# Kernel optimization log

Measured on AMD Instinct MI355X. Metric: run time of the kernel, lower is better.

## Reference

```python
import jax, jax.numpy as jnp
import numpy as np
from jax import lax

B, S, D = 2, 4096, 1024
E, H, K = 8, 2816, 2  # hidden_dim 4096 -> int(2*4096/3)=2730 -> round up to multiple_of 256 -> 2816


def setup_inputs() -> dict:
    key = jax.random.key(0)
    ks = jax.random.split(key, 5)
    scale = 0.02
    return {
        "x": jax.random.normal(ks[0], (B, S, D), dtype=jnp.float32),
        "router_w": jax.random.normal(ks[1], (E, D), dtype=jnp.float32) * scale,
        "w1": jax.random.normal(ks[2], (E, D, H), dtype=jnp.float32) * scale,
        "w2": jax.random.normal(ks[3], (E, H, D), dtype=jnp.float32) * scale,
        "w3": jax.random.normal(ks[4], (E, D, H), dtype=jnp.float32) * scale,
        "top_k": K,
    }


def reference(x, router_w, w1, w2, w3, top_k):
    b, s, d = x.shape
    e = router_w.shape[0]
    xf = x.reshape(-1, d)                                # [T, D]
    logits = xf @ router_w.T                             # [T, E]
    vals, idx = lax.top_k(logits, top_k)                 # [T, K]
    rw = jax.nn.softmax(vals.astype(jnp.float32), axis=-1).astype(x.dtype)  # [T, K]
    # combine[t, e] = routing weight of expert e for token t (0 if not selected)
    combine = jnp.sum(jax.nn.one_hot(idx, e, dtype=x.dtype) * rw[..., None], axis=1)  # [T, E]

    def body(acc, ew):
        w1e, w2e, w3e, ce = ew                           # [D,H], [H,D], [D,H], [T]
        h = jax.nn.silu(xf @ w1e) * (xf @ w3e)           # SwiGLU FFN, [T, H]
        return acc + (h @ w2e) * ce[:, None], None

    out, _ = lax.scan(body, jnp.zeros_like(xf), (w1, w2, w3, combine.T))
    return out.reshape(b, s, d)
```

## Files before the change

### kernel.cpp

```cpp
#include <hip/hip_runtime.h>
#include <stdint.h>

#define T_TOK 8192
#define DIM   1024
#define NE    8
#define NH    2816
#define NROWS (T_TOK*2)

typedef __attribute__((ext_vector_type(8))) __bf16 bf16x8;
typedef __attribute__((ext_vector_type(4))) float  f32x4;

typedef __attribute__((address_space(1))) const unsigned int g_as1;
typedef __attribute__((address_space(3))) unsigned int l_as3;
#define GLL(g, l) __builtin_amdgcn_global_load_lds((g_as1*)(g), (l_as3*)(l), 16, 0, 0)

__device__ __forceinline__ unsigned short f2bf(float f){
  union { float f; uint32_t u; } v; v.f = f;
  uint32_t r = (v.u + 0x7FFFu + ((v.u >> 16) & 1u)) >> 16;
  return (unsigned short)r;
}


__global__ void init_k(int* counts, int* cursor){
  int i = threadIdx.x;
  if (i < NE){ counts[i] = 0; cursor[i] = 0; }
}

__global__ void zero_out_k(float4* __restrict__ out){
  int i = blockIdx.x*blockDim.x + threadIdx.x;
  const int n4 = T_TOK*DIM/4;
  const float4 z = make_float4(0.f,0.f,0.f,0.f);
  for (; i < n4; i += gridDim.x*blockDim.x) out[i] = z;
}

__global__ void cvt_k(const float* __restrict__ x, unsigned short* __restrict__ xbf){
  int i = blockIdx.x*blockDim.x + threadIdx.x;
  const int total = T_TOK*DIM/8;
  for (; i < total; i += gridDim.x*blockDim.x){
    const float4 a = *(const float4*)(x + (size_t)i*8);
    const float4 b = *(const float4*)(x + (size_t)i*8 + 4);
    ushort4 lo = make_ushort4(f2bf(a.x), f2bf(a.y), f2bf(a.z), f2bf(a.w));
    ushort4 hi = make_ushort4(f2bf(b.x), f2bf(b.y), f2bf(b.z), f2bf(b.w));
    *(ushort4*)(xbf + (size_t)i*8)     = lo;
    *(ushort4*)(xbf + (size_t)i*8 + 4) = hi;
  }
}

__global__ __launch_bounds__(256) void transp_k(const float* __restrict__ in,
    unsigned short* __restrict__ outp, int R, int C)
{
  __shared__ unsigned short Tl[64*68];
  const int r0 = blockIdx.x*64, c0 = blockIdx.y*64;
  const size_t mbase = (size_t)blockIdx.z * (size_t)R * (size_t)C;
  const float* ip = in + mbase;
  unsigned short* op = outp + mbase;
  const int t = threadIdx.x;
  #pragma unroll
  for (int i=0;i<4;i++){
    const int r  = (t>>4) + i*16;
    const int cq = t & 15;
    const float4 v = *(const float4*)(ip + (size_t)(r0+r)*C + c0 + cq*4);
    Tl[(cq*4+0)*68 + r] = f2bf(v.x);
    Tl[(cq*4+1)*68 + r] = f2bf(v.y);
    Tl[(cq*4+2)*68 + r] = f2bf(v.z);
    Tl[(cq*4+3)*68 + r] = f2bf(v.w);
  }
  __syncthreads();
  #pragma unroll
  for (int i=0;i<4;i++){
    const int idx = i*1024 + t*4;
    const int c = idx>>6, r = idx&63;
    const ushort4 v = *(const ushort4*)&Tl[c*68 + r];
    *(ushort4*)(op + (size_t)(c0+c)*R + r0 + r) = v;
  }
}


__global__ void router_k(const float* __restrict__ x, const float* __restrict__ rw,
                         int* __restrict__ topk_e, float* __restrict__ topk_w,
                         int* __restrict__ counts){
  const int t = blockIdx.x;
  const int l = threadIdx.x;
  const float* xr = x + (size_t)t * DIM;
  float acc[NE];
  #pragma unroll
  for (int e=0;e<NE;e++) acc[e] = 0.f;
  #pragma unroll
  for (int i=0;i<DIM/64;i++){
    float xv = xr[l + 64*i];
    #pragma unroll
    for (int e=0;e<NE;e++) acc[e] += xv * rw[e*DIM + l + 64*i];
  }
  #pragma unroll
  for (int e=0;e<NE;e++){
    float v = acc[e];
    #pragma unroll
    for (int off=32; off; off>>=1) v += __shfl_xor(v, off);
    acc[e] = v;
  }
  if (l == 0){
    int e0 = 0; float v0 = acc[0];
    #pragma unroll
    for (int e=1;e<NE;e++) if (acc[e] > v0){ v0 = acc[e]; e0 = e; }
    int e1 = -1; float v1 = -1e30f;
    #pragma unroll
    for (int e=0;e<NE;e++) if (e != e0 && acc[e] > v1){ v1 = acc[e]; e1 = e; }
    float ex = __expf(v1 - v0);
    float s  = 1.f + ex;
    topk_e[t*2]   = e0;  topk_e[t*2+1] = e1;
    topk_w[t*2]   = 1.f/s; topk_w[t*2+1] = ex/s;
    atomicAdd(&counts[e0], 1);
    atomicAdd(&counts[e1], 1);
  }
}

__global__ void prefix_k(const int* __restrict__ counts, int* __restrict__ offs){
  if (threadIdx.x == 0 && blockIdx.x == 0){
    int s = 0;
    for (int e=0;e<NE;e++){ offs[e] = s; s += counts[e]; }
  }
}

__global__ void scatter_k(const int* __restrict__ topk_e, const float* __restrict__ topk_w,
                          const int* __restrict__ offs, int* __restrict__ cursor,
                          int* __restrict__ row_tok, float* __restrict__ row_w){
  int t = blockIdx.x*blockDim.x + threadIdx.x;
  if (t >= T_TOK) return;
  #pragma unroll
  for (int k=0;k<2;k++){
    int e = topk_e[t*2+k];
    int p = atomicAdd(&cursor[e], 1);
    int flat = offs[e] + p;
    row_tok[flat] = t;
    row_w[flat]   = topk_w[t*2+k];
  }
}


__global__ __launch_bounds__(512,2) void gemm1_bf(
    const unsigned short* __restrict__ xbf,
    const unsigned short* __restrict__ w1t, const unsigned short* __restrict__ w3t,
    unsigned short* __restrict__ hbuf,
    const int* __restrict__ row_tok,
    const int* __restrict__ counts, const int* __restrict__ offs)
{
  __shared__ unsigned short Al [2][128*32];
  __shared__ unsigned short B1l[2][128*32];
  __shared__ unsigned short B3l[2][128*32];

  const int e   = blockIdx.y >> 6;
  const int rb  = blockIdx.y & 63;
  const int cnt = counts[e];
  const int row0 = rb * 128;
  if (row0 >= cnt) return;
  const int nv   = min(128, cnt - row0);
  const int base = offs[e] + row0;
  const int h0   = blockIdx.x * 128;

  const int t  = threadIdx.x;
  const int srow = t >> 2, sch = t & 3;
  const int tok = row_tok[base + min(srow, nv-1)];
  const unsigned short* asrc = xbf + (size_t)tok*DIM + sch*8;
  const unsigned short* b1s  = w1t + ((size_t)(e*NH + h0 + srow))*DIM + sch*8;
  const unsigned short* b3s  = w3t + ((size_t)(e*NH + h0 + srow))*DIM + sch*8;
  const int lo = t*16;

  const int wid = t >> 6, l = t & 63;
  const int wr = wid >> 2, wc = wid & 3;
  const int lr = l & 15,  lk = l >> 4;

  f32x4 acc1[4][2], acc3[4][2];
  #pragma unroll
  for (int m=0;m<4;m++)
    #pragma unroll
    for (int n=0;n<2;n++){ acc1[m][n] = (f32x4)0.f; acc3[m][n] = (f32x4)0.f; }

  GLL(asrc, (char*)Al [0] + lo);
  GLL(b1s,  (char*)B1l[0] + lo);
  GLL(b3s,  (char*)B3l[0] + lo);
  __syncthreads();

  for (int kk=0; kk<DIM/32; ++kk){
    const int cur = kk & 1;
    if (kk < DIM/32 - 1){
      const int k1 = (kk+1)*32;
      GLL(asrc + k1, (char*)Al [cur^1] + lo);
      GLL(b1s  + k1, (char*)B1l[cur^1] + lo);
      GLL(b3s  + k1, (char*)B3l[cur^1] + lo);
    }
    bf16x8 a[4], b1[2], b3[2];
    #pragma unroll
    for (int m=0;m<4;m++) a[m] = *(const bf16x8*)&Al[cur][(wr*64 + m*16 + lr)*32 + lk*8];
    #pragma unroll
    for (int n=0;n<2;n++){
      b1[n] = *(const bf16x8*)&B1l[cur][(wc*32 + n*16 + lr)*32 + lk*8];
      b3[n] = *(const bf16x8*)&B3l[cur][(wc*32 + n*16 + lr)*32 + lk*8];
    }
    #pragma unroll
    for (int m=0;m<4;m++)
      #pragma unroll
      for (int n=0;n<2;n++){
        acc1[m][n] = __builtin_amdgcn_mfma_f32_16x16x32_bf16(a[m], b1[n], acc1[m][n], 0,0,0);
        acc3[m][n] = __builtin_amdgcn_mfma_f32_16x16x32_bf16(a[m], b3[n], acc3[m][n], 0,0,0);
      }
    __syncthreads();
  }

  #pragma unroll
  for (int m=0;m<4;m++){
    #pragma unroll
    for (int i=0;i<4;i++){
      const int r = wr*64 + m*16 + lk*4 + i;
      if (r < nv){
        const size_t rowbase = (size_t)(base + r) * NH;
        #pragma unroll
        for (int n=0;n<2;n++){
          float z  = acc1[m][n][i];
          float p3 = acc3[m][n][i];
          float hv = (z / (1.f + __expf(-z))) * p3;
          hbuf[rowbase + h0 + wc*32 + n*16 + lr] = f2bf(hv);
        }
      }
    }
  }
}

__global__ __launch_bounds__(512,2) void gemm2_bf(
    const unsigned short* __restrict__ hbuf,
    const unsigned short* __restrict__ w2t,
    float* __restrict__ out,
    const int* __restrict__ row_tok, const float* __restrict__ row_w,
    const int* __restrict__ counts, const int* __restrict__ offs)
{
  __shared__ unsigned short Al[2][128*32];
  __shared__ unsigned short Bl[2][128*32];

  const int e   = blockIdx.y >> 6;
  const int rb  = blockIdx.y & 63;
  const int cnt = counts[e];
  const int row0 = rb * 128;
  if (row0 >= cnt) return;
  const int nv   = min(128, cnt - row0);
  const int base = offs[e] + row0;
  const int d0   = blockIdx.x * 128;

  const int t  = threadIdx.x;
  const int srow = t >> 2, sch = t & 3;
  const unsigned short* asrc = hbuf + (size_t)(base + min(srow, nv-1))*NH + sch*8;
  const unsigned short* bs   = w2t + ((size_t)(e*DIM + d0 + srow))*NH + sch*8;
  const int lo = t*16;

  const int wid = t >> 6, l = t & 63;
  const int wr = wid >> 2, wc = wid & 3;
  const int lr = l & 15,  lk = l >> 4;

  f32x4 acc[4][2];
  #pragma unroll
  for (int m=0;m<4;m++)
    #pragma unroll
    for (int n=0;n<2;n++) acc[m][n] = (f32x4)0.f;

  GLL(asrc, (char*)Al[0] + lo);
  GLL(bs,   (char*)Bl[0] + lo);
  __syncthreads();

  for (int kk=0; kk<NH/32; ++kk){
    const int cur = kk & 1;
    if (kk < NH/32 - 1){
      const int k1 = (kk+1)*32;
      GLL(asrc + k1, (char*)Al[cur^1] + lo);
      GLL(bs   + k1, (char*)Bl[cur^1] + lo);
    }
    bf16x8 a[4], b[2];
    #pragma unroll
    for (int m=0;m<4;m++) a[m] = *(const bf16x8*)&Al[cur][(wr*64 + m*16 + lr)*32 + lk*8];
    #pragma unroll
    for (int n=0;n<2;n++)  b[n] = *(const bf16x8*)&Bl[cur][(wc*32 + n*16 + lr)*32 + lk*8];
    #pragma unroll
    for (int m=0;m<4;m++)
      #pragma unroll
      for (int n=0;n<2;n++)
        acc[m][n] = __builtin_amdgcn_mfma_f32_16x16x32_bf16(a[m], b[n], acc[m][n], 0,0,0);
    __syncthreads();
  }

  #pragma unroll
  for (int m=0;m<4;m++){
    #pragma unroll
    for (int i=0;i<4;i++){
      const int r = wr*64 + m*16 + lk*4 + i;
      if (r < nv){
        const int flat = base + r;
        const int tok  = row_tok[flat];
        const float wgt = row_w[flat];
        float* orow = out + (size_t)tok * DIM + d0 + wc*32;
        #pragma unroll
        for (int n=0;n<2;n++)
          atomicAdd(&orow[n*16 + lr], acc[m][n][i] * wgt);
      }
    }
  }
}


__global__ __launch_bounds__(256) void gemm1_k(
    const unsigned short* __restrict__ xbf,
    const float* __restrict__ w1, const float* __restrict__ w3,
    unsigned short* __restrict__ hbuf,
    const int* __restrict__ row_tok,
    const int* __restrict__ counts, const int* __restrict__ offs)
{
  __shared__ unsigned short Al [128*32];
  __shared__ unsigned short B1l[128*32];
  __shared__ unsigned short B3l[128*32];
  const int e   = blockIdx.y >> 6;
  const int rb  = blockIdx.y & 63;
  const int cnt = counts[e];
  const int row0 = rb * 128;
  if (row0 >= cnt) return;
  const int nv   = min(128, cnt - row0);
  const int base = offs[e] + row0;
  const int h0   = blockIdx.x * 128;
  const int t  = threadIdx.x;
  const int ar0 = t >> 2;
  const int ac  = t & 3;
  const int tok0 = row_tok[base + min(ar0,      nv-1)];
  const int tok1 = row_tok[base + min(ar0 + 64, nv-1)];
  const size_t asrc0 = (size_t)tok0 * DIM + ac*8;
  const size_t asrc1 = (size_t)tok1 * DIM + ac*8;
  const int dg = t >> 5;
  const int hq = t & 31;
  const float* w1p = w1 + (size_t)e * DIM * NH + (size_t)(h0 + hq*4);
  const float* w3p = w3 + (size_t)e * DIM * NH + (size_t)(h0 + hq*4);
  const int wid = t >> 6, l = t & 63;
  const int wr = wid >> 1, wc = wid & 1;
  const int lr = l & 15,  lk = l >> 4;
  f32x4 acc1[4][4], acc3[4][4];
  #pragma unroll
  for (int m=0;m<4;m++)
    #pragma unroll
    for (int n=0;n<4;n++){ acc1[m][n] = (f32x4)0.f; acc3[m][n] = (f32x4)0.f; }
  for (int kk=0; kk<DIM/32; ++kk){
    const int k0 = kk*32;
    __syncthreads();
    *(uint4*)&Al[ar0*32 + ac*8]      = *(const uint4*)(xbf + asrc0 + k0);
    *(uint4*)&Al[(ar0+64)*32 + ac*8] = *(const uint4*)(xbf + asrc1 + k0);
    {
      const float4 f0 = *(const float4*)(w1p + (size_t)(k0 + dg*4 + 0)*NH);
      const float4 f1 = *(const float4*)(w1p + (size_t)(k0 + dg*4 + 1)*NH);
      const float4 f2 = *(const float4*)(w1p + (size_t)(k0 + dg*4 + 2)*NH);
      const float4 f3 = *(const float4*)(w1p + (size_t)(k0 + dg*4 + 3)*NH);
      const float* p0=(const float*)&f0; const float* p1=(const float*)&f1;
      const float* p2=(const float*)&f2; const float* p3=(const float*)&f3;
      #pragma unroll
      for (int j=0;j<4;j++){
        ushort4 pk = make_ushort4(f2bf(p0[j]), f2bf(p1[j]), f2bf(p2[j]), f2bf(p3[j]));
        *(ushort4*)&B1l[(hq*4+j)*32 + dg*4] = pk;
      }
      const float4 g0 = *(const float4*)(w3p + (size_t)(k0 + dg*4 + 0)*NH);
      const float4 g1 = *(const float4*)(w3p + (size_t)(k0 + dg*4 + 1)*NH);
      const float4 g2 = *(const float4*)(w3p + (size_t)(k0 + dg*4 + 2)*NH);
      const float4 g3 = *(const float4*)(w3p + (size_t)(k0 + dg*4 + 3)*NH);
      const float* q0=(const float*)&g0; const float* q1=(const float*)&g1;
      const float* q2=(const float*)&g2; const float* q3=(const float*)&g3;
      #pragma unroll
      for (int j=0;j<4;j++){
        ushort4 pk = make_ushort4(f2bf(q0[j]), f2bf(q1[j]), f2bf(q2[j]), f2bf(q3[j]));
        *(ushort4*)&B3l[(hq*4+j)*32 + dg*4] = pk;
      }
    }
    __syncthreads();
    bf16x8 a[4], b1[4], b3[4];
    #pragma unroll
    for (int m=0;m<4;m++) a[m] = *(const bf16x8*)&Al[(wr*64 + m*16 + lr)*32 + lk*8];
    #pragma unroll
    for (int n=0;n<4;n++){
      b1[n] = *(const bf16x8*)&B1l[(wc*64 + n*16 + lr)*32 + lk*8];
      b3[n] = *(const bf16x8*)&B3l[(wc*64 + n*16 + lr)*32 + lk*8];
    }
    #pragma unroll
    for (int m=0;m<4;m++)
      #pragma unroll
      for (int n=0;n<4;n++){
        acc1[m][n] = __builtin_amdgcn_mfma_f32_16x16x32_bf16(a[m], b1[n], acc1[m][n], 0,0,0);
        acc3[m][n] = __builtin_amdgcn_mfma_f32_16x16x32_bf16(a[m], b3[n], acc3[m][n], 0,0,0);
      }
  }
  #pragma unroll
  for (int m=0;m<4;m++){
    #pragma unroll
    for (int i=0;i<4;i++){
      const int r = wr*64 + m*16 + lk*4 + i;
      if (r < nv){
        const size_t rowbase = (size_t)(base + r) * NH;
        #pragma unroll
        for (int n=0;n<4;n++){
          float z  = acc1[m][n][i];
          float p3 = acc3[m][n][i];
          float hv = (z / (1.f + __expf(-z))) * p3;
          hbuf[rowbase + h0 + wc*64 + n*16 + lr] = f2bf(hv);
        }
      }
    }
  }
}

__global__ __launch_bounds__(256) void gemm2_k(
    const unsigned short* __restrict__ hbuf,
    const float* __restrict__ w2,
    float* __restrict__ out,
    const int* __restrict__ row_tok, const float* __restrict__ row_w,
    const int* __restrict__ counts, const int* __restrict__ offs)
{
  __shared__ unsigned short Al[128*32];
  __shared__ unsigned short Bl[128*32];
  const int e   = blockIdx.y >> 6;
  const int rb  = blockIdx.y & 63;
  const int cnt = counts[e];
  const int row0 = rb * 128;
  if (row0 >= cnt) return;
  const int nv   = min(128, cnt - row0);
  const int base = offs[e] + row0;
  const int d0   = blockIdx.x * 128;
  const int t  = threadIdx.x;
  const int ar0 = t >> 2;
  const int ac  = t & 3;
  const size_t asrc0 = (size_t)(base + min(ar0,      nv-1)) * NH + ac*8;
  const size_t asrc1 = (size_t)(base + min(ar0 + 64, nv-1)) * NH + ac*8;
  const int dg = t >> 5;
  const int hq = t & 31;
  const float* w2p = w2 + (size_t)e * NH * DIM + (size_t)(d0 + hq*4);
  const int wid = t >> 6, l = t & 63;
  const int wr = wid >> 1, wc = wid & 1;
  const int lr = l & 15,  lk = l >> 4;
  f32x4 acc[4][4];
  #pragma unroll
  for (int m=0;m<4;m++)
    #pragma unroll
    for (int n=0;n<4;n++) acc[m][n] = (f32x4)0.f;
  for (int kk=0; kk<NH/32; ++kk){
    const int k0 = kk*32;
    __syncthreads();
    *(uint4*)&Al[ar0*32 + ac*8]      = *(const uint4*)(hbuf + asrc0 + k0);
    *(uint4*)&Al[(ar0+64)*32 + ac*8] = *(const uint4*)(hbuf + asrc1 + k0);
    {
      const float4 f0 = *(const float4*)(w2p + (size_t)(k0 + dg*4 + 0)*DIM);
      const float4 f1 = *(const float4*)(w2p + (size_t)(k0 + dg*4 + 1)*DIM);
      const float4 f2 = *(const float4*)(w2p + (size_t)(k0 + dg*4 + 2)*DIM);
      const float4 f3 = *(const float4*)(w2p + (size_t)(k0 + dg*4 + 3)*DIM);
      const float* p0=(const float*)&f0; const float* p1=(const float*)&f1;
      const float* p2=(const float*)&f2; const float* p3=(const float*)&f3;
      #pragma unroll
      for (int j=0;j<4;j++){
        ushort4 pk = make_ushort4(f2bf(p0[j]), f2bf(p1[j]), f2bf(p2[j]), f2bf(p3[j]));
        *(ushort4*)&Bl[(hq*4+j)*32 + dg*4] = pk;
      }
    }
    __syncthreads();
    bf16x8 a[4], b[4];
    #pragma unroll
    for (int m=0;m<4;m++) a[m] = *(const bf16x8*)&Al[(wr*64 + m*16 + lr)*32 + lk*8];
    #pragma unroll
    for (int n=0;n<4;n++)  b[n] = *(const bf16x8*)&Bl[(wc*64 + n*16 + lr)*32 + lk*8];
    #pragma unroll
    for (int m=0;m<4;m++)
      #pragma unroll
      for (int n=0;n<4;n++)
        acc[m][n] = __builtin_amdgcn_mfma_f32_16x16x32_bf16(a[m], b[n], acc[m][n], 0,0,0);
  }
  #pragma unroll
  for (int m=0;m<4;m++){
    #pragma unroll
    for (int i=0;i<4;i++){
      const int r = wr*64 + m*16 + lk*4 + i;
      if (r < nv){
        const int flat = base + r;
        const int tok  = row_tok[flat];
        const float wgt = row_w[flat];
        float* orow = out + (size_t)tok * DIM + d0 + wc*64;
        #pragma unroll
        for (int n=0;n<4;n++)
          atomicAdd(&orow[n*16 + lr], acc[m][n][i] * wgt);
      }
    }
  }
}


extern "C" void kernel_launch(void* const* d_in, const int* in_sizes, int n_in,
                              void* d_out, int out_size, void* d_ws, size_t ws_size,
                              hipStream_t stream) {
  (void)in_sizes; (void)n_in; (void)out_size;
  const float* x   = (const float*)d_in[0];
  const float* rw  = (const float*)d_in[1];
  const float* w1  = (const float*)d_in[2];
  const float* w2  = (const float*)d_in[3];
  const float* w3  = (const float*)d_in[4];
  float* out = (float*)d_out;
  char* ws = (char*)d_ws;

  const size_t SZ_XBF  = (size_t)T_TOK*DIM*2;
  const size_t SZ_HBUF = (size_t)NROWS*NH*2;
  const size_t SZ_WT   = (size_t)NE*NH*DIM*2;
  const size_t SZ_SMALL = (size_t)NROWS*4*2 + (size_t)T_TOK*2*4*2 + 3*64*4 + 4096;
  const size_t NEED_FAST = SZ_XBF + SZ_HBUF + 2*SZ_WT + SZ_SMALL;

  if (ws_size >= NEED_FAST) {
    size_t off = 0;
    unsigned short* xbf  = (unsigned short*)(ws + off); off += SZ_XBF;
    unsigned short* hbuf = (unsigned short*)(ws + off); off += SZ_HBUF;
    unsigned short* w1t  = (unsigned short*)(ws + off); off += SZ_WT;
    unsigned short* w3t  = (unsigned short*)(ws + off); off += SZ_WT;
    unsigned short* w2t  = w1t;
    int*   row_tok = (int*)  (ws + off); off += NROWS*4;
    float* row_w   = (float*)(ws + off); off += NROWS*4;
    int*   topk_e  = (int*)  (ws + off); off += T_TOK*2*4;
    float* topk_w  = (float*)(ws + off); off += T_TOK*2*4;
    int*   counts  = (int*)  (ws + off); off += 64;
    int*   offs    = (int*)  (ws + off); off += 64;
    int*   cursor  = (int*)  (ws + off); off += 64;

    init_k    <<<1, 64, 0, stream>>>(counts, cursor);
    zero_out_k<<<2048, 256, 0, stream>>>((float4*)out);
    cvt_k     <<<2048, 256, 0, stream>>>(x, xbf);
    router_k  <<<T_TOK, 64, 0, stream>>>(x, rw, topk_e, topk_w, counts);
    prefix_k  <<<1, 64, 0, stream>>>(counts, offs);
    scatter_k <<<(T_TOK+255)/256, 256, 0, stream>>>(topk_e, topk_w, offs, cursor, row_tok, row_w);
    transp_k  <<<dim3(DIM/64, NH/64, NE), 256, 0, stream>>>(w1, w1t, DIM, NH);
    transp_k  <<<dim3(DIM/64, NH/64, NE), 256, 0, stream>>>(w3, w3t, DIM, NH);
    gemm1_bf  <<<dim3(NH/128, NE*64), 512, 0, stream>>>(xbf, w1t, w3t, hbuf, row_tok, counts, offs);
    transp_k  <<<dim3(NH/64, DIM/64, NE), 256, 0, stream>>>(w2, w2t, NH, DIM);
    gemm2_bf  <<<dim3(DIM/128, NE*64), 512, 0, stream>>>(hbuf, w2t, out, row_tok, row_w, counts, offs);
  } else {
    size_t off = 0;
    unsigned short* xbf  = (unsigned short*)(ws + off); off += SZ_XBF;
    unsigned short* hbuf = (unsigned short*)(ws + off); off += SZ_HBUF;
    int*   row_tok = (int*)  (ws + off); off += NROWS*4;
    float* row_w   = (float*)(ws + off); off += NROWS*4;
    int*   topk_e  = (int*)  (ws + off); off += T_TOK*2*4;
    float* topk_w  = (float*)(ws + off); off += T_TOK*2*4;
    int*   counts  = (int*)  (ws + off); off += 64;
    int*   offs    = (int*)  (ws + off); off += 64;
    int*   cursor  = (int*)  (ws + off); off += 64;

    init_k    <<<1, 64, 0, stream>>>(counts, cursor);
    zero_out_k<<<2048, 256, 0, stream>>>((float4*)out);
    cvt_k     <<<2048, 256, 0, stream>>>(x, xbf);
    router_k  <<<T_TOK, 64, 0, stream>>>(x, rw, topk_e, topk_w, counts);
    prefix_k  <<<1, 64, 0, stream>>>(counts, offs);
    scatter_k <<<(T_TOK+255)/256, 256, 0, stream>>>(topk_e, topk_w, offs, cursor, row_tok, row_w);
    gemm1_k   <<<dim3(NH/128, NE*64), 256, 0, stream>>>(xbf, w1, w3, hbuf, row_tok, counts, offs);
    gemm2_k   <<<dim3(DIM/128, NE*64), 256, 0, stream>>>(hbuf, w2, out, row_tok, row_w, counts, offs);
  }
}
```

Measured before the change: 775.0 us.

## Deepen GEMM pipelines with swizzled 64-wide K tiles and wider gemm2 N tile

Both grouped GEMMs now use 64-wide K tiles with an XOR-swizzled LDS layout, a triple-buffered A tile and a double-buffered B tile. Synchronisation moves to explicit vmcnt waits plus a raw barrier, and s_setprio raises wave priority around the MFMA blocks. gemm2 widens its output tile to 256 columns so each A tile is reused twice as much and half as many blocks issue atomics, at the cost of more accumulator registers. The w1 and w3 transposes are merged into one launch to cut launch overhead. The larger LDS footprint may limit occupancy.

```diff
diff --git a/kernel.cpp b/kernel.cpp
--- a/kernel.cpp
+++ b/kernel.cpp
@@ -75,6 +75,37 @@
   }
 }
 
+__global__ __launch_bounds__(256) void transp2_k(const float* __restrict__ w1,
+    const float* __restrict__ w3, unsigned short* __restrict__ w1t,
+    unsigned short* __restrict__ w3t)
+{
+  __shared__ unsigned short Tl[64*68];
+  const int r0 = blockIdx.x*64, c0 = blockIdx.y*64;
+  const int z = blockIdx.z;
+  const size_t mbase = (size_t)(z & (NE-1)) * (size_t)DIM * (size_t)NH;
+  const float* ip = (z < NE ? w1 : w3) + mbase;
+  unsigned short* op = (z < NE ? w1t : w3t) + mbase;
+  const int t = threadIdx.x;
+  #pragma unroll
+  for (int i=0;i<4;i++){
+    const int r  = (t>>4) + i*16;
+    const int cq = t & 15;
+    const float4 v = *(const float4*)(ip + (size_t)(r0+r)*NH + c0 + cq*4);
+    Tl[(cq*4+0)*68 + r] = f2bf(v.x);
+    Tl[(cq*4+1)*68 + r] = f2bf(v.y);
+    Tl[(cq*4+2)*68 + r] = f2bf(v.z);
+    Tl[(cq*4+3)*68 + r] = f2bf(v.w);
+  }
+  __syncthreads();
+  #pragma unroll
+  for (int i=0;i<4;i++){
+    const int idx = i*1024 + t*4;
+    const int c = idx>>6, r = idx&63;
+    const ushort4 v = *(const ushort4*)&Tl[c*68 + r];
+    *(ushort4*)(op + (size_t)(c0+c)*DIM + r0 + r) = v;
+  }
+}
+
 
 __global__ void router_k(const float* __restrict__ x, const float* __restrict__ rw,
                          int* __restrict__ topk_e, float* __restrict__ topk_w,
@@ -137,16 +168,16 @@
 }
 
 
-__global__ __launch_bounds__(512,2) void gemm1_bf(
+__global__ __launch_bounds__(512,2) void gemm1_t(
     const unsigned short* __restrict__ xbf,
     const unsigned short* __restrict__ w1t, const unsigned short* __restrict__ w3t,
     unsigned short* __restrict__ hbuf,
     const int* __restrict__ row_tok,
     const int* __restrict__ counts, const int* __restrict__ offs)
 {
-  __shared__ unsigned short Al [2][128*32];
-  __shared__ unsigned short B1l[2][128*32];
-  __shared__ unsigned short B3l[2][128*32];
+  __shared__ unsigned short As [3][128*64];
+  __shared__ unsigned short B1s[2][128*64];
+  __shared__ unsigned short B3s[2][128*64];
 
   const int e   = blockIdx.y >> 6;
   const int rb  = blockIdx.y & 63;
@@ -156,18 +187,25 @@
   const int nv   = min(128, cnt - row0);
   const int base = offs[e] + row0;
   const int h0   = blockIdx.x * 128;
-
-  const int t  = threadIdx.x;
-  const int srow = t >> 2, sch = t & 3;
-  const int tok = row_tok[base + min(srow, nv-1)];
-  const unsigned short* asrc = xbf + (size_t)tok*DIM + sch*8;
-  const unsigned short* b1s  = w1t + ((size_t)(e*NH + h0 + srow))*DIM + sch*8;
-  const unsigned short* b3s  = w3t + ((size_t)(e*NH + h0 + srow))*DIM + sch*8;
-  const int lo = t*16;
+  const int NK   = DIM/64;
+
+  const int t = threadIdx.x;
+  const int r_loc = t >> 3, sct = t & 7;
+  const int csw = ((sct ^ (r_loc & 7)) << 3);
+  const int tokA0 = row_tok[base + min(r_loc,      nv-1)];
+  const int tokA1 = row_tok[base + min(64 + r_loc, nv-1)];
+  const unsigned short* aP0 = xbf + (size_t)tokA0*DIM + csw;
+  const unsigned short* aP1 = xbf + (size_t)tokA1*DIM + csw;
+  const unsigned short* b1P0 = w1t + ((size_t)(e*NH + h0) + r_loc)*DIM + csw;
+  const unsigned short* b1P1 = b1P0 + (size_t)64*DIM;
+  const unsigned short* b3P0 = w3t + ((size_t)(e*NH + h0) + r_loc)*DIM + csw;
+  const unsigned short* b3P1 = b3P0 + (size_t)64*DIM;
+  const int lo0 = t*16, lo1 = 8192 + t*16;
 
   const int wid = t >> 6, l = t & 63;
   const int wr = wid >> 2, wc = wid & 3;
   const int lr = l & 15,  lk = l >> 4;
+  const int cx0 = ((lk ^ (lr & 7)) << 3);
 
   f32x4 acc1[4][2], acc3[4][2];
   #pragma unroll
@@ -175,35 +213,54 @@
     #pragma unroll
     for (int n=0;n<2;n++){ acc1[m][n] = (f32x4)0.f; acc3[m][n] = (f32x4)0.f; }
 
-  GLL(asrc, (char*)Al [0] + lo);
-  GLL(b1s,  (char*)B1l[0] + lo);
-  GLL(b3s,  (char*)B3l[0] + lo);
-  __syncthreads();
-
-  for (int kk=0; kk<DIM/32; ++kk){
-    const int cur = kk & 1;
-    if (kk < DIM/32 - 1){
-      const int k1 = (kk+1)*32;
-      GLL(asrc + k1, (char*)Al [cur^1] + lo);
-      GLL(b1s  + k1, (char*)B1l[cur^1] + lo);
-      GLL(b3s  + k1, (char*)B3l[cur^1] + lo);
-    }
-    bf16x8 a[4], b1[2], b3[2];
-    #pragma unroll
-    for (int m=0;m<4;m++) a[m] = *(const bf16x8*)&Al[cur][(wr*64 + m*16 + lr)*32 + lk*8];
-    #pragma unroll
-    for (int n=0;n<2;n++){
-      b1[n] = *(const bf16x8*)&B1l[cur][(wc*32 + n*16 + lr)*32 + lk*8];
-      b3[n] = *(const bf16x8*)&B3l[cur][(wc*32 + n*16 + lr)*32 + lk*8];
-    }
-    #pragma unroll
-    for (int m=0;m<4;m++)
+  GLL(aP0,        (char*)As[0] + lo0);  GLL(aP1,        (char*)As[0] + lo1);
+  GLL(b1P0,       (char*)B1s[0] + lo0); GLL(b1P1,       (char*)B1s[0] + lo1);
+  GLL(b3P0,       (char*)B3s[0] + lo0); GLL(b3P1,       (char*)B3s[0] + lo1);
+  GLL(aP0 + 64,   (char*)As[1] + lo0);  GLL(aP1 + 64,   (char*)As[1] + lo1);
+
+  for (int kt = 0; kt < NK; ++kt){
+    if (kt == NK-1) { asm volatile("s_waitcnt vmcnt(0)" ::: "memory"); }
+    else            { asm volatile("s_waitcnt vmcnt(2)" ::: "memory"); }
+    __builtin_amdgcn_s_barrier();
+
+    if (kt+1 < NK){
+      const int kB = (kt+1)*64;
+      char* b1d = (char*)B1s[(kt+1)&1];
+      char* b3d = (char*)B3s[(kt+1)&1];
+      GLL(b1P0 + kB, b1d + lo0); GLL(b1P1 + kB, b1d + lo1);
+      GLL(b3P0 + kB, b3d + lo0); GLL(b3P1 + kB, b3d + lo1);
+    }
+    if (kt+2 < NK){
+      const int kA = (kt+2)*64;
+      char* ad = (char*)As[(kt+2)%3];
+      GLL(aP0 + kA, ad + lo0); GLL(aP1 + kA, ad + lo1);
+    }
+
+    const unsigned short* Ab  = As [kt%3];
+    const unsigned short* B1b = B1s[kt&1];
+    const unsigned short* B3b = B3s[kt&1];
+
+    #pragma unroll
+    for (int kk2=0; kk2<2; kk2++){
+      const int cx = cx0 ^ (kk2<<5);
+      bf16x8 a[4], b1[2], b3[2];
+      #pragma unroll
+      for (int m=0;m<4;m++) a[m] = *(const bf16x8*)&Ab[(wr*64 + m*16 + lr)*64 + cx];
       #pragma unroll
       for (int n=0;n<2;n++){
-        acc1[m][n] = __builtin_amdgcn_mfma_f32_16x16x32_bf16(a[m], b1[n], acc1[m][n], 0,0,0);
-        acc3[m][n] = __builtin_amdgcn_mfma_f32_16x16x32_bf16(a[m], b3[n], acc3[m][n], 0,0,0);
-      }
-    __syncthreads();
+        b1[n] = *(const bf16x8*)&B1b[(wc*32 + n*16 + lr)*64 + cx];
+        b3[n] = *(const bf16x8*)&B3b[(wc*32 + n*16 + lr)*64 + cx];
+      }
+      __builtin_amdgcn_s_setprio(1);
+      #pragma unroll
+      for (int m=0;m<4;m++)
+        #pragma unroll
+        for (int n=0;n<2;n++){
+          acc1[m][n] = __builtin_amdgcn_mfma_f32_16x16x32_bf16(a[m], b1[n], acc1[m][n], 0,0,0);
+          acc3[m][n] = __builtin_amdgcn_mfma_f32_16x16x32_bf16(a[m], b3[n], acc3[m][n], 0,0,0);
+        }
+      __builtin_amdgcn_s_setprio(0);
+    }
   }
 
   #pragma unroll
@@ -225,15 +282,15 @@
   }
 }
 
-__global__ __launch_bounds__(512,2) void gemm2_bf(
+__global__ __launch_bounds__(512,2) void gemm2_t(
     const unsigned short* __restrict__ hbuf,
     const unsigned short* __restrict__ w2t,
     float* __restrict__ out,
     const int* __restrict__ row_tok, const float* __restrict__ row_w,
     const int* __restrict__ counts, const int* __restrict__ offs)
 {
-  __shared__ unsigned short Al[2][128*32];
-  __shared__ unsigned short Bl[2][128*32];
+  __shared__ unsigned short As[3][128*64];
+  __shared__ unsigned short Bs[2][256*64];
 
   const int e   = blockIdx.y >> 6;
   const int rb  = blockIdx.y & 63;
@@ -242,46 +299,72 @@
   if (row0 >= cnt) return;
   const int nv   = min(128, cnt - row0);
   const int base = offs[e] + row0;
-  const int d0   = blockIdx.x * 128;
-
-  const int t  = threadIdx.x;
-  const int srow = t >> 2, sch = t & 3;
-  const unsigned short* asrc = hbuf + (size_t)(base + min(srow, nv-1))*NH + sch*8;
-  const unsigned short* bs   = w2t + ((size_t)(e*DIM + d0 + srow))*NH + sch*8;
-  const int lo = t*16;
+  const int d0   = blockIdx.x * 256;
+  const int NK   = NH/64;
+
+  const int t = threadIdx.x;
+  const int r_loc = t >> 3, sct = t & 7;
+  const int csw = ((sct ^ (r_loc & 7)) << 3);
+  const unsigned short* aP0 = hbuf + (size_t)(base + min(r_loc,      nv-1))*NH + csw;
+  const unsigned short* aP1 = hbuf + (size_t)(base + min(64 + r_loc, nv-1))*NH + csw;
+  const unsigned short* bP0 = w2t + ((size_t)(e*DIM + d0) + r_loc)*NH + csw;
+  const unsigned short* bP1 = bP0 + (size_t)64*NH;
+  const unsigned short* bP2 = bP0 + (size_t)128*NH;
+  const unsigned short* bP3 = bP0 + (size_t)192*NH;
+  const int lo0 = t*16, lo1 = 8192 + t*16, lo2 = 16384 + t*16, lo3 = 24576 + t*16;
 
   const int wid = t >> 6, l = t & 63;
   const int wr = wid >> 2, wc = wid & 3;
   const int lr = l & 15,  lk = l >> 4;
-
-  f32x4 acc[4][2];
+  const int cx0 = ((lk ^ (lr & 7)) << 3);
+
+  f32x4 acc[4][4];
   #pragma unroll
   for (int m=0;m<4;m++)
     #pragma unroll
-    for (int n=0;n<2;n++) acc[m][n] = (f32x4)0.f;
-
-  GLL(asrc, (char*)Al[0] + lo);
-  GLL(bs,   (char*)Bl[0] + lo);
-  __syncthreads();
-
-  for (int kk=0; kk<NH/32; ++kk){
-    const int cur = kk & 1;
-    if (kk < NH/32 - 1){
-      const int k1 = (kk+1)*32;
-      GLL(asrc + k1, (char*)Al[cur^1] + lo);
-      GLL(bs   + k1, (char*)Bl[cur^1] + lo);
-    }
-    bf16x8 a[4], b[2];
-    #pragma unroll
-    for (int m=0;m<4;m++) a[m] = *(const bf16x8*)&Al[cur][(wr*64 + m*16 + lr)*32 + lk*8];
-    #pragma unroll
-    for (int n=0;n<2;n++)  b[n] = *(const bf16x8*)&Bl[cur][(wc*32 + n*16 + lr)*32 + lk*8];
-    #pragma unroll
-    for (int m=0;m<4;m++)
-      #pragma unroll
-      for (int n=0;n<2;n++)
-        acc[m][n] = __builtin_amdgcn_mfma_f32_16x16x32_bf16(a[m], b[n], acc[m][n], 0,0,0);
-    __syncthreads();
+    for (int n=0;n<4;n++) acc[m][n] = (f32x4)0.f;
+
+  GLL(aP0,      (char*)As[0] + lo0); GLL(aP1,      (char*)As[0] + lo1);
+  GLL(bP0,      (char*)Bs[0] + lo0); GLL(bP1,      (char*)Bs[0] + lo1);
+  GLL(bP2,      (char*)Bs[0] + lo2); GLL(bP3,      (char*)Bs[0] + lo3);
+  GLL(aP0 + 64, (char*)As[1] + lo0); GLL(aP1 + 64, (char*)As[1] + lo1);
+
+  for (int kt = 0; kt < NK; ++kt){
+    if (kt == NK-1) { asm volatile("s_waitcnt vmcnt(0)" ::: "memory"); }
+    else            { asm volatile("s_waitcnt vmcnt(2)" ::: "memory"); }
+    __builtin_amdgcn_s_barrier();
+
+    if (kt+1 < NK){
+      const int kB = (kt+1)*64;
+      char* bd = (char*)Bs[(kt+1)&1];
+      GLL(bP0 + kB, bd + lo0); GLL(bP1 + kB, bd + lo1);
+      GLL(bP2 + kB, bd + lo2); GLL(bP3 + kB, bd + lo3);
+    }
+    if (kt+2 < NK){
+      const int kA = (kt+2)*64;
+      char* ad = (char*)As[(kt+2)%3];
+      GLL(aP0 + kA, ad + lo0); GLL(aP1 + kA, ad + lo1);
+    }
+
+    const unsigned short* Ab = As[kt%3];
+    const unsigned short* Bb = Bs[kt&1];
+
+    #pragma unroll
+    for (int kk2=0; kk2<2; kk2++){
+      const int cx = cx0 ^ (kk2<<5);
+      bf16x8 a[4], b[4];
+      #pragma unroll
+      for (int m=0;m<4;m++) a[m] = *(const bf16x8*)&Ab[(wr*64 + m*16 + lr)*64 + cx];
+      #pragma unroll
+      for (int n=0;n<4;n++)  b[n] = *(const bf16x8*)&Bb[(wc*64 + n*16 + lr)*64 + cx];
+      __builtin_amdgcn_s_setprio(1);
+      #pragma unroll
+      for (int m=0;m<4;m++)
+        #pragma unroll
+        for (int n=0;n<4;n++)
+          acc[m][n] = __builtin_amdgcn_mfma_f32_16x16x32_bf16(a[m], b[n], acc[m][n], 0,0,0);
+      __builtin_amdgcn_s_setprio(0);
+    }
   }
 
   #pragma unroll
@@ -293,9 +376,9 @@
         const int flat = base + r;
         const int tok  = row_tok[flat];
         const float wgt = row_w[flat];
-        float* orow = out + (size_t)tok * DIM + d0 + wc*32;
+        float* orow = out + (size_t)tok * DIM + d0 + wc*64;
         #pragma unroll
-        for (int n=0;n<2;n++)
+        for (int n=0;n<4;n++)
           atomicAdd(&orow[n*16 + lr], acc[m][n][i] * wgt);
       }
     }
@@ -526,11 +609,10 @@
     router_k  <<<T_TOK, 64, 0, stream>>>(x, rw, topk_e, topk_w, counts);
     prefix_k  <<<1, 64, 0, stream>>>(counts, offs);
     scatter_k <<<(T_TOK+255)/256, 256, 0, stream>>>(topk_e, topk_w, offs, cursor, row_tok, row_w);
-    transp_k  <<<dim3(DIM/64, NH/64, NE), 256, 0, stream>>>(w1, w1t, DIM, NH);
-    transp_k  <<<dim3(DIM/64, NH/64, NE), 256, 0, stream>>>(w3, w3t, DIM, NH);
-    gemm1_bf  <<<dim3(NH/128, NE*64), 512, 0, stream>>>(xbf, w1t, w3t, hbuf, row_tok, counts, offs);
+    transp2_k <<<dim3(DIM/64, NH/64, 2*NE), 256, 0, stream>>>(w1, w3, w1t, w3t);
+    gemm1_t   <<<dim3(NH/128, NE*64), 512, 0, stream>>>(xbf, w1t, w3t, hbuf, row_tok, counts, offs);
     transp_k  <<<dim3(NH/64, DIM/64, NE), 256, 0, stream>>>(w2, w2t, NH, DIM);
-    gemm2_bf  <<<dim3(DIM/128, NE*64), 512, 0, stream>>>(hbuf, w2t, out, row_tok, row_w, counts, offs);
+    gemm2_t   <<<dim3(DIM/256, NE*64), 512, 0, stream>>>(hbuf, w2t, out, row_tok, row_w, counts, offs);
   } else {
     size_t off = 0;
     unsigned short* xbf  = (unsigned short*)(ws + off); off += SZ_XBF;
```

New measurement: 898.7 us. 1.16x slower.
